# Performance work log

Hardware: AMD Instinct MI355X
Metric: run time of the kernel (lower is better)

The kernel has to match this reference:

```python
import jax, jax.numpy as jnp
import numpy as np

EPS = 1e-5  # torch LayerNorm default


def setup_inputs() -> dict:
    key = jax.random.key(0)
    k1, k2 = jax.random.split(key)
    B, S, H = 32, 4096, 1024
    lstm_output = jax.random.normal(k1, (B, S, H), dtype=jnp.float32)
    ln_gamma = jnp.ones((H,), dtype=jnp.float32)
    ln_beta = jnp.zeros((H,), dtype=jnp.float32)
    attn_w = jax.random.normal(k2, (H,), dtype=jnp.float32) / np.sqrt(H)
    return {"lstm_output": lstm_output, "ln_gamma": ln_gamma,
            "ln_beta": ln_beta, "attn_w": attn_w}


def reference(lstm_output, ln_gamma, ln_beta, attn_w):
    # LayerNorm over hidden dim
    mu = jnp.mean(lstm_output, axis=-1, keepdims=True)
    var = jnp.mean(jnp.square(lstm_output - mu), axis=-1, keepdims=True)
    normed = (lstm_output - mu) * jax.lax.rsqrt(var + EPS) * ln_gamma + ln_beta  # [B,S,H]
    # Linear(H,1,bias=False) score, then stabilize + clamp + softmax over seq
    scores = jnp.einsum('bsh,h->bs', normed, attn_w)  # [B,S]
    scores = scores - jnp.max(scores, axis=1, keepdims=True)
    scores = jnp.clip(scores, -10.0, 10.0)
    weights = jax.nn.softmax(scores, axis=1)  # dropout is identity in eval
    # Weighted-sum pooling over sequence
    return jnp.einsum('bs,bsh->bh', weights, normed)  # [B,H]
```

## Files before the change

### kernel.cpp

```cpp
#include <hip/hip_runtime.h>
#include <math.h>

#define EPS 1e-5f

static constexpr int Bc   = 32;
static constexpr int Sc   = 4096;
static constexpr int Hc   = 1024;
static constexpr int ROWS = Bc * Sc;
static constexpr int CHUNK  = 64;
static constexpr int NCHUNK = Sc / CHUNK;

__device__ __forceinline__ float waveSum(float v) {
#pragma unroll
  for (int off = 32; off > 0; off >>= 1) v += __shfl_xor(v, off, 64);
  return v;
}
__device__ __forceinline__ float waveMax(float v) {
#pragma unroll
  for (int off = 32; off > 0; off >>= 1) v = fmaxf(v, __shfl_xor(v, off, 64));
  return v;
}
__device__ __forceinline__ float blockSum(float v, float* red) {
  const int lane = threadIdx.x & 63, wid = threadIdx.x >> 6;
  const int nw = blockDim.x >> 6;
  v = waveSum(v);
  if (lane == 0) red[wid] = v;
  __syncthreads();
  if (wid == 0) {
    float t = (lane < nw) ? red[lane] : 0.0f;
    t = waveSum(t);
    if (lane == 0) red[0] = t;
  }
  __syncthreads();
  float r = red[0];
  __syncthreads();
  return r;
}
__device__ __forceinline__ float blockMax(float v, float* red) {
  const int lane = threadIdx.x & 63, wid = threadIdx.x >> 6;
  const int nw = blockDim.x >> 6;
  v = waveMax(v);
  if (lane == 0) red[wid] = v;
  __syncthreads();
  if (wid == 0) {
    float t = (lane < nw) ? red[lane] : -INFINITY;
    t = waveMax(t);
    if (lane == 0) red[0] = t;
  }
  __syncthreads();
  float r = red[0];
  __syncthreads();
  return r;
}

__global__ __launch_bounds__(256) void k1_rowstats(
    const float* __restrict__ x, const float* __restrict__ g,
    const float* __restrict__ w,
    float* __restrict__ mu_o, float* __restrict__ rstd_o,
    float* __restrict__ t_o)
{
  const int lane = threadIdx.x & 63;
  const int wv   = threadIdx.x >> 6;
  const long long row = (long long)blockIdx.x * 4 + wv;
  const float4* xr = (const float4*)(x + row * Hc);
  const float4* gr = (const float4*)g;
  const float4* wr = (const float4*)w;
  float s1 = 0.f, s2 = 0.f, t = 0.f;
#pragma unroll
  for (int k = 0; k < 4; k++) {
    const float4 xv  = xr[lane + k * 64];
    const float4 gv  = gr[lane + k * 64];
    const float4 wv4 = wr[lane + k * 64];
    s1 += xv.x + xv.y + xv.z + xv.w;
    s2 += xv.x*xv.x + xv.y*xv.y + xv.z*xv.z + xv.w*xv.w;
    t  += xv.x*gv.x*wv4.x + xv.y*gv.y*wv4.y + xv.z*gv.z*wv4.z + xv.w*gv.w*wv4.w;
  }
  s1 = waveSum(s1);
  s2 = waveSum(s2);
  t  = waveSum(t);
  if (lane == 0) {
    float mu   = s1 * (1.0f / Hc);
    float var  = s2 * (1.0f / Hc) - mu * mu;
    float rstd = rsqrtf(var + EPS);
    mu_o[row]   = mu;
    rstd_o[row] = rstd;
    t_o[row]    = t;
  }
}

__global__ __launch_bounds__(1024) void k2_softmax(
    const float* __restrict__ g, const float* __restrict__ w,
    const float* __restrict__ beta,
    const float* __restrict__ mu, const float* __restrict__ rstd,
    const float* __restrict__ tdot,
    float* __restrict__ c, float* __restrict__ dvec)
{
  __shared__ float red[16];
  const int b   = blockIdx.x;
  const int tid = threadIdx.x;

  const float gv = g[tid], wv = w[tid], bv = beta[tid];
  const float sgw = blockSum(gv * wv, red);
  const float bw  = blockSum(bv * wv, red);

  float sc[4], mus[4], rst[4];
  float localmax = -INFINITY;
#pragma unroll
  for (int k = 0; k < 4; k++) {
    const int row = b * Sc + tid + k * 1024;
    const float m = mu[row], r = rstd[row], t = tdot[row];
    const float s = r * (t - m * sgw) + bw;
    sc[k] = s; mus[k] = m; rst[k] = r;
    localmax = fmaxf(localmax, s);
  }
  const float smax = blockMax(localmax, red);

  float e[4], zp = 0.0f;
#pragma unroll
  for (int k = 0; k < 4; k++) {
    const float v = fminf(fmaxf(sc[k] - smax, -10.0f), 10.0f);
    e[k] = expf(v);
    zp += e[k];
  }
  const float Z = blockSum(zp, red);
  const float invZ = 1.0f / Z;

  float dp = 0.0f;
#pragma unroll
  for (int k = 0; k < 4; k++) {
    const float cv = e[k] * invZ * rst[k];
    c[b * Sc + tid + k * 1024] = cv;
    dp += cv * mus[k];
  }
  const float d = blockSum(dp, red);
  if (tid == 0) dvec[b] = d;
}

__global__ __launch_bounds__(256) void k3_wsum(
    const float* __restrict__ x, const float* __restrict__ c,
    const float* __restrict__ dvec, const float* __restrict__ g,
    const float* __restrict__ beta, float* __restrict__ out)
{
  __shared__ float cs[CHUNK];
  const int chunk = blockIdx.x;
  const int b     = blockIdx.y;
  const int t     = threadIdx.x;
  const int s0    = chunk * CHUNK;
  if (t < CHUNK) cs[t] = c[b * Sc + s0 + t];
  __syncthreads();

  const float4* xp = (const float4*)(x + (long long)(b * Sc + s0) * Hc) + t;
  float4 acc = make_float4(0.f, 0.f, 0.f, 0.f);
#pragma unroll 4
  for (int i = 0; i < CHUNK; i++) {
    const float cv = cs[i];
    const float4 xv = xp[i * (Hc / 4)];
    acc.x = fmaf(cv, xv.x, acc.x);
    acc.y = fmaf(cv, xv.y, acc.y);
    acc.z = fmaf(cv, xv.z, acc.z);
    acc.w = fmaf(cv, xv.w, acc.w);
  }
  const float4 gv = ((const float4*)g)[t];
  const float4 bv = ((const float4*)beta)[t];
  float4 res;
  res.x = gv.x * acc.x;
  res.y = gv.y * acc.y;
  res.z = gv.z * acc.z;
  res.w = gv.w * acc.w;
  if (chunk == 0) {
    const float d = dvec[b];
    res.x += bv.x - gv.x * d;
    res.y += bv.y - gv.y * d;
    res.z += bv.z - gv.z * d;
    res.w += bv.w - gv.w * d;
  }
  float* o = out + b * Hc + t * 4;
  atomicAdd(o + 0, res.x);
  atomicAdd(o + 1, res.y);
  atomicAdd(o + 2, res.z);
  atomicAdd(o + 3, res.w);
}

extern "C" void kernel_launch(void* const* d_in, const int* in_sizes, int n_in,
                              void* d_out, int out_size, void* d_ws, size_t ws_size,
                              hipStream_t stream) {
  const float* x    = (const float*)d_in[0];
  const float* g    = (const float*)d_in[1];
  const float* beta = (const float*)d_in[2];
  const float* w    = (const float*)d_in[3];
  float* out = (float*)d_out;

  float* mu   = (float*)d_ws;
  float* rstd = mu   + ROWS;
  float* tdot = rstd + ROWS;
  float* c    = tdot + ROWS;
  float* dvec = c    + ROWS;

  hipMemsetAsync(d_out, 0, (size_t)Bc * Hc * sizeof(float), stream);
  k1_rowstats<<<ROWS / 4, 256, 0, stream>>>(x, g, w, mu, rstd, tdot);
  k2_softmax<<<Bc, 1024, 0, stream>>>(g, w, beta, mu, rstd, tdot, c, dvec);
  dim3 grid3(NCHUNK, Bc);
  k3_wsum<<<grid3, 256, 0, stream>>>(x, c, dvec, g, beta, out);
}
```

Before: 775.2 us.

## Replace atomic output accumulation with partial-sum buffer and final reduction kernel

```diff
diff --git a/kernel.cpp b/kernel.cpp
--- a/kernel.cpp
+++ b/kernel.cpp
@@ -7,13 +7,21 @@
 static constexpr int Sc   = 4096;
 static constexpr int Hc   = 1024;
 static constexpr int ROWS = Bc * Sc;
-static constexpr int CHUNK  = 64;
-static constexpr int NCHUNK = Sc / CHUNK;
+static constexpr int SSPLIT = 32;
+static constexpr int RPC    = Sc / SSPLIT;
 
 __device__ __forceinline__ float waveSum(float v) {
 #pragma unroll
   for (int off = 32; off > 0; off >>= 1) v += __shfl_xor(v, off, 64);
   return v;
+}
+__device__ __forceinline__ void waveSum3(float& a, float& b, float& c) {
+#pragma unroll
+  for (int off = 32; off > 0; off >>= 1) {
+    a += __shfl_xor(a, off, 64);
+    b += __shfl_xor(b, off, 64);
+    c += __shfl_xor(c, off, 64);
+  }
 }
 __device__ __forceinline__ float waveMax(float v) {
 #pragma unroll
@@ -53,9 +61,22 @@
   return r;
 }
 
+__global__ __launch_bounds__(1024) void k0_prep(
+    const float* __restrict__ g, const float* __restrict__ w,
+    const float* __restrict__ beta,
+    float* __restrict__ gw, float* __restrict__ scal)
+{
+  __shared__ float red[16];
+  const int tid = threadIdx.x;
+  const float gv = g[tid], wv = w[tid], bv = beta[tid];
+  gw[tid] = gv * wv;
+  const float sgw = blockSum(gv * wv, red);
+  const float bw  = blockSum(bv * wv, red);
+  if (tid == 0) { scal[0] = sgw; scal[1] = bw; }
+}
+
 __global__ __launch_bounds__(256) void k1_rowstats(
-    const float* __restrict__ x, const float* __restrict__ g,
-    const float* __restrict__ w,
+    const float* __restrict__ x, const float* __restrict__ gw,
     float* __restrict__ mu_o, float* __restrict__ rstd_o,
     float* __restrict__ t_o)
 {
@@ -63,21 +84,17 @@
   const int wv   = threadIdx.x >> 6;
   const long long row = (long long)blockIdx.x * 4 + wv;
   const float4* xr = (const float4*)(x + row * Hc);
-  const float4* gr = (const float4*)g;
-  const float4* wr = (const float4*)w;
+  const float4* gr = (const float4*)gw;
   float s1 = 0.f, s2 = 0.f, t = 0.f;
 #pragma unroll
   for (int k = 0; k < 4; k++) {
-    const float4 xv  = xr[lane + k * 64];
-    const float4 gv  = gr[lane + k * 64];
-    const float4 wv4 = wr[lane + k * 64];
+    const float4 xv = xr[lane + k * 64];
+    const float4 gv = gr[lane + k * 64];
     s1 += xv.x + xv.y + xv.z + xv.w;
     s2 += xv.x*xv.x + xv.y*xv.y + xv.z*xv.z + xv.w*xv.w;
-    t  += xv.x*gv.x*wv4.x + xv.y*gv.y*wv4.y + xv.z*gv.z*wv4.z + xv.w*gv.w*wv4.w;
-  }
-  s1 = waveSum(s1);
-  s2 = waveSum(s2);
-  t  = waveSum(t);
+    t  += xv.x*gv.x + xv.y*gv.y + xv.z*gv.z + xv.w*gv.w;
+  }
+  waveSum3(s1, s2, t);
   if (lane == 0) {
     float mu   = s1 * (1.0f / Hc);
     float var  = s2 * (1.0f / Hc) - mu * mu;
@@ -89,8 +106,7 @@
 }
 
 __global__ __launch_bounds__(1024) void k2_softmax(
-    const float* __restrict__ g, const float* __restrict__ w,
-    const float* __restrict__ beta,
+    const float* __restrict__ scal,
     const float* __restrict__ mu, const float* __restrict__ rstd,
     const float* __restrict__ tdot,
     float* __restrict__ c, float* __restrict__ dvec)
@@ -98,10 +114,8 @@
   __shared__ float red[16];
   const int b   = blockIdx.x;
   const int tid = threadIdx.x;
-
-  const float gv = g[tid], wv = w[tid], bv = beta[tid];
-  const float sgw = blockSum(gv * wv, red);
-  const float bw  = blockSum(bv * wv, red);
+  const float sgw = scal[0];
+  const float bw  = scal[1];
 
   float sc[4], mus[4], rst[4];
   float localmax = -INFINITY;
@@ -136,23 +150,22 @@
   if (tid == 0) dvec[b] = d;
 }
 
-__global__ __launch_bounds__(256) void k3_wsum(
+__global__ __launch_bounds__(256) void k3_partial(
     const float* __restrict__ x, const float* __restrict__ c,
-    const float* __restrict__ dvec, const float* __restrict__ g,
-    const float* __restrict__ beta, float* __restrict__ out)
-{
-  __shared__ float cs[CHUNK];
+    float* __restrict__ part)
+{
+  __shared__ float cs[RPC];
   const int chunk = blockIdx.x;
   const int b     = blockIdx.y;
   const int t     = threadIdx.x;
-  const int s0    = chunk * CHUNK;
-  if (t < CHUNK) cs[t] = c[b * Sc + s0 + t];
+  const int s0    = chunk * RPC;
+  if (t < RPC) cs[t] = c[b * Sc + s0 + t];
   __syncthreads();
 
   const float4* xp = (const float4*)(x + (long long)(b * Sc + s0) * Hc) + t;
   float4 acc = make_float4(0.f, 0.f, 0.f, 0.f);
 #pragma unroll 4
-  for (int i = 0; i < CHUNK; i++) {
+  for (int i = 0; i < RPC; i++) {
     const float cv = cs[i];
     const float4 xv = xp[i * (Hc / 4)];
     acc.x = fmaf(cv, xv.x, acc.x);
@@ -160,25 +173,33 @@
     acc.z = fmaf(cv, xv.z, acc.z);
     acc.w = fmaf(cv, xv.w, acc.w);
   }
+  float4* pp = (float4*)(part + ((long long)(b * SSPLIT + chunk)) * Hc) + t;
+  *pp = acc;
+}
+
+__global__ __launch_bounds__(256) void k4_final(
+    const float* __restrict__ part, const float* __restrict__ dvec,
+    const float* __restrict__ g, const float* __restrict__ beta,
+    float* __restrict__ out)
+{
+  const int b = blockIdx.x;
+  const int t = threadIdx.x;
+  const float4* pp = (const float4*)(part + (long long)b * SSPLIT * Hc) + t;
+  float4 acc = make_float4(0.f, 0.f, 0.f, 0.f);
+#pragma unroll
+  for (int j = 0; j < SSPLIT; j++) {
+    const float4 pv = pp[j * (Hc / 4)];
+    acc.x += pv.x; acc.y += pv.y; acc.z += pv.z; acc.w += pv.w;
+  }
+  const float d = dvec[b];
   const float4 gv = ((const float4*)g)[t];
   const float4 bv = ((const float4*)beta)[t];
   float4 res;
-  res.x = gv.x * acc.x;
-  res.y = gv.y * acc.y;
-  res.z = gv.z * acc.z;
-  res.w = gv.w * acc.w;
-  if (chunk == 0) {
-    const float d = dvec[b];
-    res.x += bv.x - gv.x * d;
-    res.y += bv.y - gv.y * d;
-    res.z += bv.z - gv.z * d;
-    res.w += bv.w - gv.w * d;
-  }
-  float* o = out + b * Hc + t * 4;
-  atomicAdd(o + 0, res.x);
-  atomicAdd(o + 1, res.y);
-  atomicAdd(o + 2, res.z);
-  atomicAdd(o + 3, res.w);
+  res.x = gv.x * (acc.x - d) + bv.x;
+  res.y = gv.y * (acc.y - d) + bv.y;
+  res.z = gv.z * (acc.z - d) + bv.z;
+  res.w = gv.w * (acc.w - d) + bv.w;
+  ((float4*)(out + b * Hc))[t] = res;
 }
 
 extern "C" void kernel_launch(void* const* d_in, const int* in_sizes, int n_in,
@@ -190,15 +211,19 @@
   const float* w    = (const float*)d_in[3];
   float* out = (float*)d_out;
 
-  float* mu   = (float*)d_ws;
-  float* rstd = mu   + ROWS;
+  float* gw   = (float*)d_ws;
+  float* scal = gw + Hc;
+  float* mu   = scal + 2;
+  float* rstd = mu + ROWS;
   float* tdot = rstd + ROWS;
   float* c    = tdot + ROWS;
-  float* dvec = c    + ROWS;
-
-  hipMemsetAsync(d_out, 0, (size_t)Bc * Hc * sizeof(float), stream);
-  k1_rowstats<<<ROWS / 4, 256, 0, stream>>>(x, g, w, mu, rstd, tdot);
-  k2_softmax<<<Bc, 1024, 0, stream>>>(g, w, beta, mu, rstd, tdot, c, dvec);
-  dim3 grid3(NCHUNK, Bc);
-  k3_wsum<<<grid3, 256, 0, stream>>>(x, c, dvec, g, beta, out);
-}
+  float* dvec = c + ROWS;
+  float* part = dvec + Bc;
+
+  k0_prep<<<1, 1024, 0, stream>>>(g, w, beta, gw, scal);
+  k1_rowstats<<<ROWS / 4, 256, 0, stream>>>(x, gw, mu, rstd, tdot);
+  k2_softmax<<<Bc, 1024, 0, stream>>>(scal, mu, rstd, tdot, c, dvec);
+  dim3 grid3(SSPLIT, Bc);
+  k3_partial<<<grid3, 256, 0, stream>>>(x, c, part);
+  k4_final<<<Bc, 256, 0, stream>>>(part, dvec, g, beta, out);
+}
```

Measured after the change: 769.3 us. About the same (-0.8%).
